# Optimization experiments

Measured on AMD Instinct MI355X. Metric: run time of the kernel, lower is better.

The kernel has to match this reference:

```python
import jax, jax.numpy as jnp
import numpy as np

N_AGENTS = 32
UNIT_DIM = 64
HIDDEN = 128
BATCH = 1024
STATE_DIM = 128


def setup_inputs() -> dict:
    key = jax.random.key(0)
    ks = jax.random.split(key, 8)
    s = 0.05
    return {
        "state": jax.random.normal(ks[0], (BATCH, STATE_DIM), dtype=jnp.float32),
        "unit_states": jax.random.normal(ks[1], (N_AGENTS, BATCH, UNIT_DIM), dtype=jnp.float32),
        # edge_predictor params, stored [in, out] so y = x @ W + b (matches torch Linear math)
        "W1": jax.random.normal(ks[2], (2 * UNIT_DIM, HIDDEN), dtype=jnp.float32) * s,
        "b1": jnp.zeros((HIDDEN,), dtype=jnp.float32),
        "W2": jax.random.normal(ks[3], (HIDDEN, HIDDEN), dtype=jnp.float32) * s,
        "b2": jnp.zeros((HIDDEN,), dtype=jnp.float32),
        "W3": jax.random.normal(ks[4], (HIDDEN, 1), dtype=jnp.float32) * s,
        "b3": jnp.zeros((1,), dtype=jnp.float32),
    }


def reference(state, unit_states, W1, b1, W2, b2, W3, b3):
    # unit_states: [n_agents, B, d] -> [B, n_agents, d]  (permute(1,0,2))
    us = jnp.transpose(unit_states, (1, 0, 2))
    d = us.shape[-1]
    # Pairwise concat [us_i, us_j] through the first Linear is equivalent to
    # splitting W1 into its i-half and j-half and broadcast-adding (same math,
    # avoids materializing the [B,n,n,2d] concat tensor). Dropout rate is 0.0
    # (eval-mode identity).
    hi = us @ W1[:d]   # [B, n, H]
    hj = us @ W1[d:]   # [B, n, H]
    h = jax.nn.relu(hi[:, :, None, :] + hj[:, None, :, :] + b1)  # [B, n, n, H]
    h = jax.nn.relu(h @ W2 + b2)                                  # [B, n, n, H]
    logits = (h @ W3 + b3)[..., 0]                                # [B, n, n]
    adj = jax.nn.sigmoid(logits)
    # graph_add_self_loop = True
    adj = adj + jnp.eye(adj.shape[-1], dtype=adj.dtype)[None]
    return adj
```

## Files before the change

kernel.cpp:

```cpp
#include <hip/hip_runtime.h>
#include <hip/hip_bf16.h>

#define BATCH 1024
#define NA 32
#define UD 64
#define HID 128

typedef _Float16 f16x8 __attribute__((ext_vector_type(8)));
typedef float f32x4 __attribute__((ext_vector_type(4)));
typedef float f32x16 __attribute__((ext_vector_type(16)));

__global__ void prep_weights(const float* __restrict__ W1,
                             const float* __restrict__ W2,
                             _Float16* __restrict__ ws)
{
    int tid  = blockIdx.x * blockDim.x + threadIdx.x;
    int unit = tid >> 6;
    int lane = tid & 63;
    f16x8 v;
    if (unit < 32) {
        int m  = unit >> 3, ks = unit & 7;
        int h  = m * 32 + (lane & 31);
        int k0 = ks * 16 + (lane >> 5) * 8;
        #pragma unroll
        for (int e = 0; e < 8; ++e)
            v[e] = (_Float16)W2[(k0 + e) * HID + h];
    } else {
        int u = unit - 32;
        int hh = u >> 4, ks = (u >> 3) & 1, nt = u & 7;
        int col = nt * 16 + (lane & 15);
        int k0  = ks * 32 + (lane >> 4) * 8;
        #pragma unroll
        for (int e = 0; e < 8; ++e)
            v[e] = (_Float16)W1[(hh * UD + k0 + e) * HID + col];
    }
    *(f16x8*)&ws[(size_t)(unit * 64 + lane) * 8] = v;
}

__global__ __launch_bounds__(256, 2)
void graph_learner_kernel(const float* __restrict__ us_g,
                          const float* __restrict__ b1,
                          const float* __restrict__ b2,
                          const float* __restrict__ W3,
                          const float* __restrict__ b3,
                          const _Float16* __restrict__ ws,
                          float* __restrict__ out)
{
    __shared__ _Float16 us_f16[NA * UD]  __attribute__((aligned(16)));
    __shared__ _Float16 hi_lds[NA * HID] __attribute__((aligned(16)));
    __shared__ _Float16 hj_lds[NA * HID] __attribute__((aligned(16)));
    __shared__ _Float16 w2_lds[32 * 64 * 8] __attribute__((aligned(16)));
    __shared__ float    w3_lds[HID] __attribute__((aligned(16)));

    const int b    = blockIdx.x;
    const int t    = threadIdx.x;
    const int w    = t >> 6;
    const int lane = t & 63;
    const int l15  = lane & 15;
    const int lq   = lane >> 4;
    const int l31  = lane & 31;
    const int hi2  = lane >> 5;

    {
        int i  = t >> 3;
        int c  = t & 7;
        const float* src = us_g + ((size_t)i * BATCH + (size_t)b) * UD + c * 8;
        float4 va = *(const float4*)src;
        float4 vb = *(const float4*)(src + 4);
        f16x8 v8;
        v8[0] = (_Float16)va.x; v8[1] = (_Float16)va.y;
        v8[2] = (_Float16)va.z; v8[3] = (_Float16)va.w;
        v8[4] = (_Float16)vb.x; v8[5] = (_Float16)vb.y;
        v8[6] = (_Float16)vb.z; v8[7] = (_Float16)vb.w;
        *(f16x8*)&us_f16[i * UD + ((c ^ (i & 7)) << 3)] = v8;
    }

    {
        const f16x8* src = (const f16x8*)ws;
        f16x8*       dst = (f16x8*)w2_lds;
        #pragma unroll
        for (int q = 0; q < 8; ++q) {
            int s = q * 256 + t;
            dst[s] = src[s];
        }
    }
    if (t < 32)
        *(f32x4*)&w3_lds[t * 4] = *(const f32x4*)&W3[t * 4];

    f32x16 b2q[4];
    #pragma unroll
    for (int m = 0; m < 4; ++m)
        #pragma unroll
        for (int g = 0; g < 4; ++g) {
            f32x4 v = *(const f32x4*)&b2[m * 32 + g * 8 + hi2 * 4];
            #pragma unroll
            for (int s = 0; s < 4; ++s)
                b2q[m][g * 4 + s] = v[s];
        }
    const float b3s = b3[0];

    const int Mt = w >> 1;
    const int nh = w & 1;
    f16x8 w1f[4][2][2];
    float b1v[4];
    #pragma unroll
    for (int n = 0; n < 4; ++n) {
        int nt = nh * 4 + n;
        b1v[n] = b1[nt * 16 + l15];
        #pragma unroll
        for (int h = 0; h < 2; ++h)
            #pragma unroll
            for (int ks = 0; ks < 2; ++ks) {
                int u = 32 + h * 16 + ks * 8 + nt;
                w1f[n][h][ks] = *(const f16x8*)&ws[(size_t)(u * 64 + lane) * 8];
            }
    }

    __syncthreads();

    {
        f16x8 af[2];
        #pragma unroll
        for (int ks = 0; ks < 2; ++ks) {
            int row = Mt * 16 + l15;
            int c   = ks * 4 + lq;
            af[ks] = *(const f16x8*)&us_f16[row * UD + ((c ^ (row & 7)) << 3)];
        }
        #pragma unroll
        for (int n = 0; n < 4; ++n) {
            int nt = nh * 4 + n;
            f32x4 ahi = {b1v[n], b1v[n], b1v[n], b1v[n]};
            f32x4 ahj = {0.f, 0.f, 0.f, 0.f};
            #pragma unroll
            for (int ks = 0; ks < 2; ++ks) {
                ahi = __builtin_amdgcn_mfma_f32_16x16x32_f16(af[ks], w1f[n][0][ks], ahi, 0, 0, 0);
                ahj = __builtin_amdgcn_mfma_f32_16x16x32_f16(af[ks], w1f[n][1][ks], ahj, 0, 0, 0);
            }
            #pragma unroll
            for (int r = 0; r < 4; ++r) {
                int row = Mt * 16 + lq * 4 + r;
                int col = nt * 16 + l15;
                int idx = row * HID + ((((col >> 3) ^ (row & 15)) << 3) + (col & 7));
                hi_lds[idx] = (_Float16)ahi[r];
                hj_lds[idx] = (_Float16)ahj[r];
            }
        }
    }

    __syncthreads();

    const _Float16* hjr = &hj_lds[l31 * HID];
    const int jsz = l31 & 15;

    #pragma unroll 1
    for (int tt = 0; tt < 8; ++tt) {
        asm volatile("" ::: "memory");
        const int i   = w + tt * 4;
        const int isz = i & 15;
        const _Float16* hir = &hi_lds[i * HID];

        f32x16 acc[4];
        #pragma unroll
        for (int ks = 0; ks < 8; ++ks) {
            int c = ks * 2 + hi2;
            f16x8 h8 = *(const f16x8*)&hir[(c ^ isz) << 3];
            f16x8 g8 = *(const f16x8*)&hjr[(c ^ jsz) << 3];
            f16x8 s  = h8 + g8;
            f16x8 z  = {};
            f16x8 xb = __builtin_elementwise_max(s, z);
            #pragma unroll
            for (int m = 0; m < 4; ++m) {
                f16x8 wf = *(const f16x8*)&w2_lds[(size_t)((m * 8 + ks) * 64 + lane) * 8];
                acc[m] = __builtin_amdgcn_mfma_f32_32x32x16_f16(
                    wf, xb, (ks == 0) ? b2q[m] : acc[m], 0, 0, 0);
            }
        }

        float pa = 0.f, pb = 0.f;
        #pragma unroll
        for (int m = 0; m < 4; ++m)
            #pragma unroll
            for (int g = 0; g < 4; ++g) {
                f32x4 w3v = *(const f32x4*)&w3_lds[m * 32 + g * 8 + hi2 * 4];
                pa += fmaxf(acc[m][g * 4 + 0], 0.f) * w3v[0];
                pb += fmaxf(acc[m][g * 4 + 1], 0.f) * w3v[1];
                pa += fmaxf(acc[m][g * 4 + 2], 0.f) * w3v[2];
                pb += fmaxf(acc[m][g * 4 + 3], 0.f) * w3v[3];
            }
        float p = pa + pb;
        p += __shfl_xor(p, 32);

        float x  = p + b3s;
        float sg = 1.f / (1.f + __expf(-x));
        if (l31 == i) sg += 1.f;
        if (lane < 32)
            out[(size_t)b * (NA * NA) + i * 32 + l31] = sg;
    }
}

extern "C" void kernel_launch(void* const* d_in, const int* in_sizes, int n_in,
                              void* d_out, int out_size, void* d_ws, size_t ws_size,
                              hipStream_t stream) {
    const float* us = (const float*)d_in[1];
    const float* W1 = (const float*)d_in[2];
    const float* b1 = (const float*)d_in[3];
    const float* W2 = (const float*)d_in[4];
    const float* b2 = (const float*)d_in[5];
    const float* W3 = (const float*)d_in[6];
    const float* b3 = (const float*)d_in[7];
    float* out = (float*)d_out;
    _Float16* ws = (_Float16*)d_ws;

    prep_weights<<<dim3(16), dim3(256), 0, stream>>>(W1, W2, ws);
    graph_learner_kernel<<<dim3(BATCH), dim3(256), 0, stream>>>(
        us, b1, b2, W3, b3, ws, out);
}
```

Before: 119.3 us.

## Split hidden dim across waves with register-resident W2 and cross-wave logit reduction

Each wave now owns one 32-wide slice of the second layer's hidden dimension and keeps its W2 fragments, b2 and W3 slices in registers. It loops over all 32 i rows instead of 8. The hj row is also loaded into registers once. Per-wave partial logits are written to a small LDS buffer and summed after a barrier, then sigmoid and the self-loop are applied with coalesced stores. This removes the 32 KB W2 LDS staging and the per-MFMA LDS weight reads, in exchange for more hi row reads and an extra reduction pass.

```diff
diff --git a/kernel.cpp b/kernel.cpp
--- a/kernel.cpp
+++ b/kernel.cpp
@@ -49,8 +49,7 @@
     __shared__ _Float16 us_f16[NA * UD]  __attribute__((aligned(16)));
     __shared__ _Float16 hi_lds[NA * HID] __attribute__((aligned(16)));
     __shared__ _Float16 hj_lds[NA * HID] __attribute__((aligned(16)));
-    __shared__ _Float16 w2_lds[32 * 64 * 8] __attribute__((aligned(16)));
-    __shared__ float    w3_lds[HID] __attribute__((aligned(16)));
+    __shared__ float    pw_lds[NA * NA * 4] __attribute__((aligned(16)));
 
     const int b    = blockIdx.x;
     const int t    = threadIdx.x;
@@ -75,29 +74,23 @@
         *(f16x8*)&us_f16[i * UD + ((c ^ (i & 7)) << 3)] = v8;
     }
 
-    {
-        const f16x8* src = (const f16x8*)ws;
-        f16x8*       dst = (f16x8*)w2_lds;
-        #pragma unroll
-        for (int q = 0; q < 8; ++q) {
-            int s = q * 256 + t;
-            dst[s] = src[s];
-        }
-    }
-    if (t < 32)
-        *(f32x4*)&w3_lds[t * 4] = *(const f32x4*)&W3[t * 4];
-
-    f32x16 b2q[4];
-    #pragma unroll
-    for (int m = 0; m < 4; ++m)
-        #pragma unroll
-        for (int g = 0; g < 4; ++g) {
-            f32x4 v = *(const f32x4*)&b2[m * 32 + g * 8 + hi2 * 4];
-            #pragma unroll
-            for (int s = 0; s < 4; ++s)
-                b2q[m][g * 4 + s] = v[s];
-        }
+    float b2q[16], w3q[16];
+    #pragma unroll
+    for (int g = 0; g < 4; ++g) {
+        f32x4 vb2 = *(const f32x4*)&b2[w * 32 + g * 8 + hi2 * 4];
+        f32x4 vw3 = *(const f32x4*)&W3[w * 32 + g * 8 + hi2 * 4];
+        #pragma unroll
+        for (int s = 0; s < 4; ++s) {
+            b2q[g * 4 + s] = vb2[s];
+            w3q[g * 4 + s] = vw3[s];
+        }
+    }
     const float b3s = b3[0];
+
+    f16x8 w2f[8];
+    #pragma unroll
+    for (int ks = 0; ks < 8; ++ks)
+        w2f[ks] = *(const f16x8*)&ws[(size_t)((w * 8 + ks) * 64 + lane) * 8];
 
     const int Mt = w >> 1;
     const int nh = w & 1;
@@ -149,52 +142,60 @@
 
     __syncthreads();
 
-    const _Float16* hjr = &hj_lds[l31 * HID];
-    const int jsz = l31 & 15;
+    f16x8 g8[8];
+    #pragma unroll
+    for (int ks = 0; ks < 8; ++ks) {
+        int c = ks * 2 + hi2;
+        g8[ks] = *(const f16x8*)&hj_lds[l31 * HID + ((c ^ (l31 & 15)) << 3)];
+    }
 
     #pragma unroll 1
-    for (int tt = 0; tt < 8; ++tt) {
-        asm volatile("" ::: "memory");
-        const int i   = w + tt * 4;
+    for (int i = 0; i < 32; ++i) {
         const int isz = i & 15;
         const _Float16* hir = &hi_lds[i * HID];
 
-        f32x16 acc[4];
+        f16x8 h8[8];
         #pragma unroll
         for (int ks = 0; ks < 8; ++ks) {
             int c = ks * 2 + hi2;
-            f16x8 h8 = *(const f16x8*)&hir[(c ^ isz) << 3];
-            f16x8 g8 = *(const f16x8*)&hjr[(c ^ jsz) << 3];
-            f16x8 s  = h8 + g8;
+            h8[ks] = *(const f16x8*)&hir[(c ^ isz) << 3];
+        }
+
+        f32x16 acc;
+        #pragma unroll
+        for (int ks = 0; ks < 8; ++ks) {
+            f16x8 s  = h8[ks] + g8[ks];
             f16x8 z  = {};
             f16x8 xb = __builtin_elementwise_max(s, z);
-            #pragma unroll
-            for (int m = 0; m < 4; ++m) {
-                f16x8 wf = *(const f16x8*)&w2_lds[(size_t)((m * 8 + ks) * 64 + lane) * 8];
-                acc[m] = __builtin_amdgcn_mfma_f32_32x32x16_f16(
-                    wf, xb, (ks == 0) ? b2q[m] : acc[m], 0, 0, 0);
-            }
-        }
-
-        float pa = 0.f, pb = 0.f;
-        #pragma unroll
-        for (int m = 0; m < 4; ++m)
-            #pragma unroll
-            for (int g = 0; g < 4; ++g) {
-                f32x4 w3v = *(const f32x4*)&w3_lds[m * 32 + g * 8 + hi2 * 4];
-                pa += fmaxf(acc[m][g * 4 + 0], 0.f) * w3v[0];
-                pb += fmaxf(acc[m][g * 4 + 1], 0.f) * w3v[1];
-                pa += fmaxf(acc[m][g * 4 + 2], 0.f) * w3v[2];
-                pb += fmaxf(acc[m][g * 4 + 3], 0.f) * w3v[3];
-            }
-        float p = pa + pb;
+            if (ks == 0) {
+                f32x16 c0;
+                #pragma unroll
+                for (int r = 0; r < 16; ++r) c0[r] = b2q[r];
+                acc = __builtin_amdgcn_mfma_f32_32x32x16_f16(w2f[0], xb, c0, 0, 0, 0);
+            } else {
+                acc = __builtin_amdgcn_mfma_f32_32x32x16_f16(w2f[ks], xb, acc, 0, 0, 0);
+            }
+        }
+
+        float p = 0.f;
+        #pragma unroll
+        for (int r = 0; r < 16; ++r)
+            p += fmaxf(acc[r], 0.f) * w3q[r];
         p += __shfl_xor(p, 32);
-
-        float x  = p + b3s;
+        if (lane < 32)
+            pw_lds[(i * 32 + l31) * 4 + w] = p;
+    }
+
+    __syncthreads();
+
+    #pragma unroll
+    for (int q = 0; q < 4; ++q) {
+        int p = q * 256 + t;
+        f32x4 v = *(const f32x4*)&pw_lds[p * 4];
+        float x  = v[0] + v[1] + v[2] + v[3] + b3s;
         float sg = 1.f / (1.f + __expf(-x));
-        if (l31 == i) sg += 1.f;
-        if (lane < 32)
-            out[(size_t)b * (NA * NA) + i * 32 + l31] = sg;
+        if ((p >> 5) == (p & 31)) sg += 1.f;
+        out[(size_t)b * (NA * NA) + p] = sg;
     }
 }
 
```

Measured after the change: 119.9 us. About the same (+0.5%).
